# Performance work log

Hardware: AMD Instinct MI355X
Metric: run time of the kernel (lower is better)

The kernel has to match this reference:

```python
import jax, jax.numpy as jnp
import numpy as np

N_NODES = 50000
D_FEAT = 128
N_EDGES = 800000
C = 1.0  # curvature (init kwarg)
MIN_NORM = 1e-15
ARTANH_EPS = 1e-15


def logmap0(x, c):
    # PoincareBall.logmap0: x/(sqrt(c)||x||) * artanh(sqrt(c)||x||), with the
    # same clamping as the torch repo (norm clamped to MIN_NORM, artanh arg to 1-eps).
    sqrt_c = c ** 0.5
    x_norm = jnp.maximum(jnp.linalg.norm(x, axis=-1, keepdims=True), MIN_NORM)
    u = jnp.clip(sqrt_c * x_norm, -1.0 + ARTANH_EPS, 1.0 - ARTANH_EPS)
    return x * (jnp.arctanh(u) / (sqrt_c * x_norm))


def setup_inputs() -> dict:
    key = jax.random.key(0)
    k1, k2, k3, k4 = jax.random.split(key, 4)
    # scale into the Poincare ball (||x|| < 1/sqrt(c))
    x = jax.random.normal(k1, (N_NODES, D_FEAT), dtype=jnp.float32) * 1e-3
    adj_rows = jax.random.randint(k2, (N_EDGES,), 0, N_NODES, dtype=jnp.int32)
    adj_cols = jax.random.randint(k3, (N_EDGES,), 0, N_NODES, dtype=jnp.int32)
    adj_vals = jax.random.uniform(k4, (N_EDGES,), dtype=jnp.float32)
    return {"x": x, "adj_rows": adj_rows, "adj_cols": adj_cols, "adj_vals": adj_vals}


def reference(x, adj_rows, adj_cols, adj_vals) -> jnp.ndarray:
    x_tangent = logmap0(x, C)                       # [N, d] elementwise hyperbolic map
    gathered = adj_vals[:, None] * x_tangent[adj_cols]  # [E, d] edge-parallel gather
    support_t = jax.ops.segment_sum(gathered, adj_rows, num_segments=N_NODES)  # [N, d]
    return support_t
```

## Files before the change

kernel.cpp:

```cpp
#include <hip/hip_runtime.h>
#include <math.h>

#define D_FEAT 128
#define CAP 32
#define OCAP 4096

typedef float  v2f __attribute__((ext_vector_type(2)));
typedef int    v2i __attribute__((ext_vector_type(2)));
typedef float  v4f __attribute__((ext_vector_type(4)));
typedef unsigned v4u __attribute__((ext_vector_type(4)));

static __device__ inline unsigned short f2bf(float f) {
    unsigned u = __float_as_uint(f);
    u += 0x7FFFu + ((u >> 16) & 1u);
    return (unsigned short)(u >> 16);
}

__global__ void __launch_bounds__(256)
scatter_scale_kernel(const float* __restrict__ x,
                     unsigned short* __restrict__ xt,
                     const int* __restrict__ rows,
                     const int* __restrict__ cols,
                     const float* __restrict__ vals,
                     int* __restrict__ cnt,
                     int* __restrict__ buckets,
                     int* __restrict__ ocount,
                     int4* __restrict__ oedges,
                     int n_nodes, int n_edges,
                     int n_scatter_blocks) {
    if ((int)blockIdx.x < n_scatter_blocks) {
        const int base = blockIdx.x * 2048 + threadIdx.x;
        int   r[8]; int cc[8]; float vv[8]; bool ok[8]; int slot[8];
        #pragma unroll
        for (int k = 0; k < 8; ++k) {
            int e = base + k * 256;
            ok[k] = e < n_edges;
            r[k]  = ok[k] ? __builtin_nontemporal_load(rows + e) : 0;
            cc[k] = ok[k] ? __builtin_nontemporal_load(cols + e) : 0;
            vv[k] = ok[k] ? __builtin_nontemporal_load(vals + e) : 0.0f;
        }
        #pragma unroll
        for (int k = 0; k < 8; ++k)
            slot[k] = ok[k] ? atomicAdd(&cnt[r[k]], 1) : 0;
        #pragma unroll
        for (int k = 0; k < 8; ++k) {
            if (ok[k]) {
                v2i p;
                p.x = cc[k];
                p.y = __float_as_int(vv[k]);
                if (slot[k] < CAP) {
                    *((v2i*)(buckets + 2 * ((size_t)r[k] * CAP + slot[k]))) = p;
                } else {
                    int o = atomicAdd(ocount, 1);
                    if (o < OCAP) {
                        int4 q; q.x = r[k]; q.y = p.x; q.z = p.y; q.w = 0;
                        oedges[o] = q;
                    }
                }
            }
        }
    } else {
        const int lane = threadIdx.x & 63;
        const int wave = threadIdx.x >> 6;
        const int row = ((int)blockIdx.x - n_scatter_blocks) * 4 + wave;
        if (row >= n_nodes) return;

        v2f v = __builtin_nontemporal_load(
            (const v2f*)(x + (size_t)row * D_FEAT) + lane);
        float ss = v.x * v.x + v.y * v.y;
        #pragma unroll
        for (int off = 32; off > 0; off >>= 1)
            ss += __shfl_xor(ss, off, 64);

        float norm = sqrtf(ss);
        float nc = fmaxf(norm, 1e-15f);
        float u = fminf(nc, 1.0f - 1e-15f);
        float at = 0.5f * (log1pf(u) - log1pf(-u));
        float s = at / nc;

        unsigned packed = (unsigned)f2bf(v.x * s) |
                          ((unsigned)f2bf(v.y * s) << 16);
        __builtin_nontemporal_store(
            packed, (unsigned*)(xt + (size_t)row * D_FEAT) + lane);
    }
}

__global__ void __launch_bounds__(256)
gather_bucket_kernel(const unsigned short* __restrict__ xt,
                     const int* __restrict__ cnt,
                     const int* __restrict__ buckets,
                     float* __restrict__ out, int n_nodes) {
    const int lane = threadIdx.x & 63;
    const int wave = threadIdx.x >> 6;
    const int row = blockIdx.x * 4 + wave;
    if (row >= n_nodes) return;

    int deg = cnt[row];
    deg = deg < CAP ? deg : CAP;

    v2i myp = {0, 0};
    if (lane < deg)
        myp = ((const v2i*)(buckets + 2 * (size_t)row * CAP))[lane];
    int pc = myp.x;
    float pw = __int_as_float(myp.y);

    const int g = lane >> 4;
    const int t = lane & 15;

    float a0 = 0, a1 = 0, a2 = 0, a3 = 0, a4 = 0, a5 = 0, a6 = 0, a7 = 0;

    for (int j = 0; j < deg; j += 8) {
        int i0 = j + g, i1 = j + 4 + g;
        int i0c = i0 < deg ? i0 : 0;
        int i1c = i1 < deg ? i1 : 0;
        int c0 = __shfl(pc, i0c, 64);
        int c1 = __shfl(pc, i1c, 64);
        float w0 = __shfl(pw, i0c, 64);
        float w1 = __shfl(pw, i1c, 64);
        if (i0 >= deg) w0 = 0.0f;
        if (i1 >= deg) w1 = 0.0f;
        v4u u0 = ((const v4u*)(xt + ((size_t)c0 << 7)))[t];
        v4u u1 = ((const v4u*)(xt + ((size_t)c1 << 7)))[t];
        a0 = fmaf(w0, __uint_as_float(u0.x << 16), a0);
        a1 = fmaf(w0, __uint_as_float(u0.x & 0xFFFF0000u), a1);
        a2 = fmaf(w0, __uint_as_float(u0.y << 16), a2);
        a3 = fmaf(w0, __uint_as_float(u0.y & 0xFFFF0000u), a3);
        a4 = fmaf(w0, __uint_as_float(u0.z << 16), a4);
        a5 = fmaf(w0, __uint_as_float(u0.z & 0xFFFF0000u), a5);
        a6 = fmaf(w0, __uint_as_float(u0.w << 16), a6);
        a7 = fmaf(w0, __uint_as_float(u0.w & 0xFFFF0000u), a7);
        a0 = fmaf(w1, __uint_as_float(u1.x << 16), a0);
        a1 = fmaf(w1, __uint_as_float(u1.x & 0xFFFF0000u), a1);
        a2 = fmaf(w1, __uint_as_float(u1.y << 16), a2);
        a3 = fmaf(w1, __uint_as_float(u1.y & 0xFFFF0000u), a3);
        a4 = fmaf(w1, __uint_as_float(u1.z << 16), a4);
        a5 = fmaf(w1, __uint_as_float(u1.z & 0xFFFF0000u), a5);
        a6 = fmaf(w1, __uint_as_float(u1.w << 16), a6);
        a7 = fmaf(w1, __uint_as_float(u1.w & 0xFFFF0000u), a7);
    }

    a0 += __shfl_xor(a0, 16, 64); a0 += __shfl_xor(a0, 32, 64);
    a1 += __shfl_xor(a1, 16, 64); a1 += __shfl_xor(a1, 32, 64);
    a2 += __shfl_xor(a2, 16, 64); a2 += __shfl_xor(a2, 32, 64);
    a3 += __shfl_xor(a3, 16, 64); a3 += __shfl_xor(a3, 32, 64);
    a4 += __shfl_xor(a4, 16, 64); a4 += __shfl_xor(a4, 32, 64);
    a5 += __shfl_xor(a5, 16, 64); a5 += __shfl_xor(a5, 32, 64);
    a6 += __shfl_xor(a6, 16, 64); a6 += __shfl_xor(a6, 32, 64);
    a7 += __shfl_xor(a7, 16, 64); a7 += __shfl_xor(a7, 32, 64);

    if (g == 0) {
        v4f* op = (v4f*)(out + ((size_t)row << 7) + t * 8);
        v4f o0; o0.x = a0; o0.y = a1; o0.z = a2; o0.w = a3;
        v4f o1; o1.x = a4; o1.y = a5; o1.z = a6; o1.w = a7;
        __builtin_nontemporal_store(o0, op);
        __builtin_nontemporal_store(o1, op + 1);
    }
}

__global__ void cleanup_kernel(const unsigned short* __restrict__ xt,
                               const int* __restrict__ ocount,
                               const int4* __restrict__ oedges,
                               float* __restrict__ out) {
    int tt = blockIdx.x * blockDim.x + threadIdx.x;
    int e = tt >> 5, sub = tt & 31;
    int n = *ocount;
    n = n < OCAP ? n : OCAP;
    if (e >= n) return;
    int4 q = oedges[e];
    float w = __int_as_float(q.z);
    const unsigned* xr = (const unsigned*)(xt + ((size_t)q.y << 7));
    unsigned u0 = xr[sub * 2], u1 = xr[sub * 2 + 1];
    float* o = out + ((size_t)q.x << 7) + sub * 4;
    atomicAdd(o + 0, w * __uint_as_float(u0 << 16));
    atomicAdd(o + 1, w * __uint_as_float(u0 & 0xFFFF0000u));
    atomicAdd(o + 2, w * __uint_as_float(u1 << 16));
    atomicAdd(o + 3, w * __uint_as_float(u1 & 0xFFFF0000u));
}

__global__ void fallback_kernel(const float* __restrict__ x,
                                const int* __restrict__ rows,
                                const int* __restrict__ cols,
                                const float* __restrict__ vals,
                                float* __restrict__ out, int n_edges) {
    int gid = blockIdx.x * blockDim.x + threadIdx.x;
    int e = gid >> 5, t = gid & 31;
    if (e >= n_edges) return;
    int c = cols[e];
    const float* xr = x + (size_t)c * D_FEAT;
    float ss = 0.0f;
    for (int i = 0; i < D_FEAT; ++i) ss += xr[i] * xr[i];
    float nc = fmaxf(sqrtf(ss), 1e-15f);
    float u = fminf(nc, 1.0f - 1e-15f);
    float w = vals[e] * (0.5f * (log1pf(u) - log1pf(-u))) / nc;
    const float4* xc = (const float4*)xr;
    float4 xv = xc[t];
    float* o = out + (size_t)rows[e] * D_FEAT + t * 4;
    atomicAdd(o + 0, w * xv.x);
    atomicAdd(o + 1, w * xv.y);
    atomicAdd(o + 2, w * xv.z);
    atomicAdd(o + 3, w * xv.w);
}


extern "C" void kernel_launch(void* const* d_in, const int* in_sizes, int n_in,
                              void* d_out, int out_size, void* d_ws, size_t ws_size,
                              hipStream_t stream) {
    const float* x    = (const float*)d_in[0];
    const int*   rows = (const int*)d_in[1];
    const int*   cols = (const int*)d_in[2];
    const float* vals = (const float*)d_in[3];
    float* out = (float*)d_out;

    const int n_nodes = in_sizes[0] / D_FEAT;
    const int n_edges = in_sizes[1];

    char* wsb = (char*)d_ws;
    const int n_scatter_blocks = (n_edges + 2047) / 2048;
    const int n_scale_blocks   = (n_nodes + 3) / 4;

    size_t xt_bytes    = (size_t)n_nodes * D_FEAT * 2;
    size_t cnt_off     = xt_bytes;
    size_t ocount_off  = cnt_off + (size_t)n_nodes * 4;
    size_t oedges_off  = (ocount_off + 4 + 255) & ~(size_t)255;
    size_t buckets_off = (oedges_off + (size_t)OCAP * 16 + 511) & ~(size_t)511;
    size_t need        = buckets_off + (size_t)n_nodes * CAP * 8;

    if (ws_size >= need) {
        unsigned short* xt = (unsigned short*)wsb;
        int*  cnt     = (int*)(wsb + cnt_off);
        int*  ocount  = (int*)(wsb + ocount_off);
        int4* oedges  = (int4*)(wsb + oedges_off);
        int*  buckets = (int*)(wsb + buckets_off);

        hipMemsetAsync(cnt, 0, ocount_off + 4 - cnt_off, stream);
        scatter_scale_kernel<<<n_scatter_blocks + n_scale_blocks, 256, 0, stream>>>(
            x, xt, rows, cols, vals, cnt, buckets, ocount, oedges,
            n_nodes, n_edges, n_scatter_blocks);
        gather_bucket_kernel<<<(n_nodes + 3) / 4, 256, 0, stream>>>(
            xt, cnt, buckets, out, n_nodes);
        cleanup_kernel<<<(OCAP * 32) / 256, 256, 0, stream>>>(xt, ocount, oedges, out);
    } else {
        hipMemsetAsync(out, 0, (size_t)out_size * sizeof(float), stream);
        long long total = (long long)n_edges * 32;
        fallback_kernel<<<(int)((total + 255) / 256), 256, 0, stream>>>(
            x, rows, cols, vals, out, n_edges);
    }
}
```

Before: 169.7 us.

## Shard per-row edge counters and fold overflow edges into gather kernel

Splits each row's counter and bucket into four shards chosen by thread index, which spreads same-row atomics across separate counters. The gather kernel compacts the valid shard entries through ballot, popcount and shared memory. Overflow edges are now handled inside the gather kernel by rows whose shard overflowed, each scanning the overflow list, so the separate atomic cleanup launch is gone. In exchange, the bucket span grows to 48 slots per row, raising workspace and memset size, and an overflowing row does a linear scan of the overflow list.

```diff
diff --git a/kernel.cpp b/kernel.cpp
--- a/kernel.cpp
+++ b/kernel.cpp
@@ -2,7 +2,9 @@
 #include <math.h>
 
 #define D_FEAT 128
-#define CAP 32
+#define NSH 4
+#define SC 12
+#define SPAN (NSH * SC)
 #define OCAP 4096
 
 typedef float  v2f __attribute__((ext_vector_type(2)));
@@ -26,30 +28,32 @@
                      int* __restrict__ buckets,
                      int* __restrict__ ocount,
                      int4* __restrict__ oedges,
-                     int n_nodes, int n_edges,
+                     int n_nodes, int n_edges, int npad,
                      int n_scatter_blocks) {
     if ((int)blockIdx.x < n_scatter_blocks) {
         const int base = blockIdx.x * 2048 + threadIdx.x;
-        int   r[8]; int cc[8]; float vv[8]; bool ok[8]; int slot[8];
+        int r[8]; int cc[8]; float vv[8]; bool ok[8]; int slot[8]; int sh[8];
         #pragma unroll
         for (int k = 0; k < 8; ++k) {
             int e = base + k * 256;
             ok[k] = e < n_edges;
+            sh[k] = (base + k) & (NSH - 1);
             r[k]  = ok[k] ? __builtin_nontemporal_load(rows + e) : 0;
             cc[k] = ok[k] ? __builtin_nontemporal_load(cols + e) : 0;
             vv[k] = ok[k] ? __builtin_nontemporal_load(vals + e) : 0.0f;
         }
         #pragma unroll
         for (int k = 0; k < 8; ++k)
-            slot[k] = ok[k] ? atomicAdd(&cnt[r[k]], 1) : 0;
+            slot[k] = ok[k] ? atomicAdd(&cnt[sh[k] * npad + r[k]], 1) : 0;
         #pragma unroll
         for (int k = 0; k < 8; ++k) {
             if (ok[k]) {
                 v2i p;
                 p.x = cc[k];
                 p.y = __float_as_int(vv[k]);
-                if (slot[k] < CAP) {
-                    *((v2i*)(buckets + 2 * ((size_t)r[k] * CAP + slot[k]))) = p;
+                if (slot[k] < SC) {
+                    *((v2i*)(buckets +
+                             2 * ((size_t)r[k] * SPAN + sh[k] * SC + slot[k]))) = p;
                 } else {
                     int o = atomicAdd(ocount, 1);
                     if (o < OCAP) {
@@ -89,20 +93,35 @@
 gather_bucket_kernel(const unsigned short* __restrict__ xt,
                      const int* __restrict__ cnt,
                      const int* __restrict__ buckets,
-                     float* __restrict__ out, int n_nodes) {
+                     const int* __restrict__ ocount,
+                     const int4* __restrict__ oedges,
+                     float* __restrict__ out, int n_nodes, int npad) {
+    __shared__ v2i comp[4][SPAN];
     const int lane = threadIdx.x & 63;
     const int wave = threadIdx.x >> 6;
     const int row = blockIdx.x * 4 + wave;
     if (row >= n_nodes) return;
 
-    int deg = cnt[row];
-    deg = deg < CAP ? deg : CAP;
-
-    v2i myp = {0, 0};
-    if (lane < deg)
-        myp = ((const v2i*)(buckets + 2 * (size_t)row * CAP))[lane];
-    int pc = myp.x;
-    float pw = __int_as_float(myp.y);
+    const bool inr = lane < SPAN;
+    const int shard = inr ? lane / SC : 0;
+    const int off   = inr ? lane - shard * SC : 0;
+    int craw = inr ? cnt[shard * npad + row] : 0;
+    int cs = craw < SC ? craw : SC;
+    const bool valid = inr && (off < cs);
+
+    v2i entry = {0, 0};
+    if (valid)
+        entry = ((const v2i*)(buckets + 2 * (size_t)row * SPAN))[lane];
+
+    unsigned long long mask = __ballot(valid);
+    int pos = (int)__popcll(mask & ((1ull << lane) - 1ull));
+    int deg = (int)__popcll(mask);
+
+    if (valid) comp[wave][pos] = entry;
+    v2i me = {0, 0};
+    if (lane < deg) me = comp[wave][lane];
+    int pc = me.x;
+    float pw = __int_as_float(me.y);
 
     const int g = lane >> 4;
     const int t = lane & 15;
@@ -139,6 +158,26 @@
         a7 = fmaf(w1, __uint_as_float(u1.w & 0xFFFF0000u), a7);
     }
 
+    if (__ballot(inr && craw > SC) != 0ull) {
+        int n = *ocount;
+        n = n < OCAP ? n : OCAP;
+        for (int j = 0; j < n; ++j) {
+            int4 q = oedges[j];
+            if (q.x == row) {
+                float w = (g == 0) ? __int_as_float(q.z) : 0.0f;
+                v4u u = ((const v4u*)(xt + ((size_t)q.y << 7)))[t];
+                a0 = fmaf(w, __uint_as_float(u.x << 16), a0);
+                a1 = fmaf(w, __uint_as_float(u.x & 0xFFFF0000u), a1);
+                a2 = fmaf(w, __uint_as_float(u.y << 16), a2);
+                a3 = fmaf(w, __uint_as_float(u.y & 0xFFFF0000u), a3);
+                a4 = fmaf(w, __uint_as_float(u.z << 16), a4);
+                a5 = fmaf(w, __uint_as_float(u.z & 0xFFFF0000u), a5);
+                a6 = fmaf(w, __uint_as_float(u.w << 16), a6);
+                a7 = fmaf(w, __uint_as_float(u.w & 0xFFFF0000u), a7);
+            }
+        }
+    }
+
     a0 += __shfl_xor(a0, 16, 64); a0 += __shfl_xor(a0, 32, 64);
     a1 += __shfl_xor(a1, 16, 64); a1 += __shfl_xor(a1, 32, 64);
     a2 += __shfl_xor(a2, 16, 64); a2 += __shfl_xor(a2, 32, 64);
@@ -155,26 +194,6 @@
         __builtin_nontemporal_store(o0, op);
         __builtin_nontemporal_store(o1, op + 1);
     }
-}
-
-__global__ void cleanup_kernel(const unsigned short* __restrict__ xt,
-                               const int* __restrict__ ocount,
-                               const int4* __restrict__ oedges,
-                               float* __restrict__ out) {
-    int tt = blockIdx.x * blockDim.x + threadIdx.x;
-    int e = tt >> 5, sub = tt & 31;
-    int n = *ocount;
-    n = n < OCAP ? n : OCAP;
-    if (e >= n) return;
-    int4 q = oedges[e];
-    float w = __int_as_float(q.z);
-    const unsigned* xr = (const unsigned*)(xt + ((size_t)q.y << 7));
-    unsigned u0 = xr[sub * 2], u1 = xr[sub * 2 + 1];
-    float* o = out + ((size_t)q.x << 7) + sub * 4;
-    atomicAdd(o + 0, w * __uint_as_float(u0 << 16));
-    atomicAdd(o + 1, w * __uint_as_float(u0 & 0xFFFF0000u));
-    atomicAdd(o + 2, w * __uint_as_float(u1 << 16));
-    atomicAdd(o + 3, w * __uint_as_float(u1 & 0xFFFF0000u));
 }
 
 __global__ void fallback_kernel(const float* __restrict__ x,
@@ -213,6 +232,7 @@
 
     const int n_nodes = in_sizes[0] / D_FEAT;
     const int n_edges = in_sizes[1];
+    const int npad = (n_nodes + 255) & ~255;
 
     char* wsb = (char*)d_ws;
     const int n_scatter_blocks = (n_edges + 2047) / 2048;
@@ -220,10 +240,10 @@
 
     size_t xt_bytes    = (size_t)n_nodes * D_FEAT * 2;
     size_t cnt_off     = xt_bytes;
-    size_t ocount_off  = cnt_off + (size_t)n_nodes * 4;
+    size_t ocount_off  = cnt_off + (size_t)NSH * npad * 4;
     size_t oedges_off  = (ocount_off + 4 + 255) & ~(size_t)255;
     size_t buckets_off = (oedges_off + (size_t)OCAP * 16 + 511) & ~(size_t)511;
-    size_t need        = buckets_off + (size_t)n_nodes * CAP * 8;
+    size_t need        = buckets_off + (size_t)n_nodes * SPAN * 8;
 
     if (ws_size >= need) {
         unsigned short* xt = (unsigned short*)wsb;
@@ -235,10 +255,9 @@
         hipMemsetAsync(cnt, 0, ocount_off + 4 - cnt_off, stream);
         scatter_scale_kernel<<<n_scatter_blocks + n_scale_blocks, 256, 0, stream>>>(
             x, xt, rows, cols, vals, cnt, buckets, ocount, oedges,
-            n_nodes, n_edges, n_scatter_blocks);
+            n_nodes, n_edges, npad, n_scatter_blocks);
         gather_bucket_kernel<<<(n_nodes + 3) / 4, 256, 0, stream>>>(
-            xt, cnt, buckets, out, n_nodes);
-        cleanup_kernel<<<(OCAP * 32) / 256, 256, 0, stream>>>(xt, ocount, oedges, out);
+            xt, cnt, buckets, ocount, oedges, out, n_nodes, npad);
     } else {
         hipMemsetAsync(out, 0, (size_t)out_size * sizeof(float), stream);
         long long total = (long long)n_edges * 32;
```

New measurement: 170.1 us. Within noise of the previous version (+0.2%).
